# Kernel optimization log

Measured on AMD Instinct MI355X. Metric: run time of the kernel, lower is better.

## Reference

```python
import jax, jax.numpy as jnp
import numpy as np

N, E = 100_000, 1_600_000
C_IN = C_OUT = 2


def _ln(h, g, b, eps=1e-5):
    mu = h.mean(-1, keepdims=True)
    var = ((h - mu) ** 2).mean(-1, keepdims=True)
    return (h - mu) * jax.lax.rsqrt(var + eps) * g + b


def _radial(x, W1, b1, g1, be1, W2, b2, g2, be2, W3, b3):
    h = jax.nn.relu(_ln(x @ W1 + b1, g1, be1))
    h = jax.nn.relu(_ln(h @ W2 + b2, g2, be2))
    return h @ W3 + b3


def setup_inputs() -> dict:
    key = jax.random.key(0)
    ks = jax.random.split(key, 20)
    inp = {
        "f0": jax.random.normal(ks[0], (N, C_IN, 1), jnp.float32),
        "f1": jax.random.normal(ks[1], (N, C_IN, 3), jnp.float32),
        "dist": jax.random.uniform(ks[2], (E,), jnp.float32),
        "u": jax.random.randint(ks[3], (E,), 0, N),
        "v": jax.random.randint(ks[4], (E,), 0, N),
        "wq": 0.5 * jax.random.normal(ks[5], (2, C_OUT, C_IN), jnp.float32),
        "wj00": jax.random.normal(ks[6], (E, 1, 1, 1), jnp.float32),
        "wj01": jax.random.normal(ks[7], (E, 1, 1, 3), jnp.float32),
        "wj10": jax.random.normal(ks[8], (E, 1, 3, 1), jnp.float32),
        "wj11": jax.random.normal(ks[9], (E, 3, 3, 3), jnp.float32),
        # radial MLP params for the 4 WLayers, index i = 2*l + k
        "rW1": 0.5 * jax.random.normal(ks[10], (4, C_IN + 1, 16), jnp.float32),
        "rb1": jnp.zeros((4, 16), jnp.float32),
        "g1": jnp.ones((4, 16), jnp.float32),
        "be1": jnp.zeros((4, 16), jnp.float32),
        "rW2": 0.3 * jax.random.normal(ks[11], (4, 16, 16), jnp.float32),
        "rb2": jnp.zeros((4, 16), jnp.float32),
        "g2": jnp.ones((4, 16), jnp.float32),
        "be2": jnp.zeros((4, 16), jnp.float32),
        "W3_00": 0.3 * jax.random.normal(ks[12], (16, 4), jnp.float32),
        "b3_00": jnp.zeros((4,), jnp.float32),
        "W3_01": 0.3 * jax.random.normal(ks[13], (16, 4), jnp.float32),
        "b3_01": jnp.zeros((4,), jnp.float32),
        "W3_10": 0.3 * jax.random.normal(ks[14], (16, 4), jnp.float32),
        "b3_10": jnp.zeros((4,), jnp.float32),
        "W3_11": 0.3 * jax.random.normal(ks[15], (16, 12), jnp.float32),
        "b3_11": jnp.zeros((12,), jnp.float32),
    }
    return inp


def reference(f0, f1, dist, u, v, wq, wj00, wj01, wj10, wj11,
              rW1, rb1, g1, be1, rW2, rb2, g2, be2,
              W3_00, b3_00, W3_01, b3_01, W3_10, b3_10, W3_11, b3_11):
    n = f0.shape[0]
    e = u.shape[0]
    # calc_q: [N, c_out, sum(2k+1)=4]
    q = jnp.concatenate([jnp.einsum('oi,nik->nok', wq[0], f0),
                         jnp.einsum('oi,nik->nok', wq[1], f1)], axis=2)
    # per-edge radial input: [dot(f0_src, f0_dst) over rep dim, dist] -> [E, c_in+1]
    vec = jnp.concatenate([jnp.sum(f0[u] * f0[v], axis=2), dist[:, None]], axis=1)
    f_dst = (f0[v], f1[v])  # edges.dst[k]
    wjs = {(0, 0): wj00, (0, 1): wj01, (1, 0): wj10, (1, 1): wj11}
    W3s = {(0, 0): (W3_00, b3_00), (0, 1): (W3_01, b3_01),
           (1, 0): (W3_10, b3_10), (1, 1): (W3_11, b3_11)}
    # calc_k: for each output degree l, sum over input degrees k of
    #   einsum('ejoi,ejlk,eik->eol', R, w_j, f_dst[k])  (fused form of the
    #   original 'ejoi,ejlk->eoilk' then 'eoilk,eik->eol')
    kl = []
    for l in range(2):
        acc = jnp.zeros((e, C_OUT, 2 * l + 1), f0.dtype)
        for k in range(2):
            i = 2 * l + k
            W3, b3 = W3s[(l, k)]
            J = 2 * min(k, l) + 1
            R = _radial(vec, rW1[i], rb1[i], g1[i], be1[i],
                        rW2[i], rb2[i], g2[i], be2[i], W3, b3)
            R = R.reshape(e, J, C_OUT, C_IN)
            acc = acc + jnp.einsum('ejoi,ejlk,eik->eol', R, wjs[(l, k)], f_dst[k])
        kl.append(acc)
    k_feat = jnp.concatenate(kl, axis=2)  # [E, c_out, 4]
    dot = jnp.einsum('eol,eol->e', q[v], k_feat)  # [E]
    # scatter logsumexp over destination nodes, then edge softmax weights
    m = jax.lax.stop_gradient(jax.ops.segment_max(dot, v, num_segments=n))
    m = jnp.where(jnp.isfinite(m), m, 0.0)
    ssum = jax.ops.segment_sum(jnp.exp(dot - m[v]), v, num_segments=n)
    lse = m + jnp.log(ssum)
    return jnp.exp(dot - lse[v])
```

## Files before the change

kernel.cpp:

```cpp
#include <hip/hip_runtime.h>
#include <math.h>


#define TPB 256

typedef float f2 __attribute__((ext_vector_type(2)));

static __device__ __forceinline__ f2 fma2(f2 a, f2 b, f2 c) {
    return __builtin_elementwise_fma(a, b, c);
}
static __device__ __forceinline__ f2 splat(float x) {
    f2 r;
    r.x = x;
    r.y = x;
    return r;
}
static __device__ __forceinline__ float get16(const f2* h, int c) {
    return (c & 1) ? h[c >> 1].y : h[c >> 1].x;
}

static __device__ __forceinline__ void ln_relu16(f2* h, const float* __restrict__ g,
                                                 const float* __restrict__ be) {
    const f2* g2 = (const f2*)g;
    const f2* be2 = (const f2*)be;
    f2 s = h[0] + h[1] + h[2] + h[3] + h[4] + h[5] + h[6] + h[7];
    const float mu = (s.x + s.y) * 0.0625f;
    const f2 mu2 = splat(mu);
    f2 vs = splat(0.f);
#pragma unroll
    for (int i = 0; i < 8; ++i) {
        f2 d = h[i] - mu2;
        vs = fma2(d, d, vs);
    }
    const float var = (vs.x + vs.y) * 0.0625f;
    const f2 r2 = splat(rsqrtf(var + 1e-5f));
    const f2 zero = splat(0.f);
#pragma unroll
    for (int i = 0; i < 8; ++i) {
        f2 t = (h[i] - mu2) * r2;
        h[i] = __builtin_elementwise_max(fma2(t, g2[i], be2[i]), zero);
    }
}

static __device__ __forceinline__ void radial_h2(
    float v0, float v1, float v2, const float* __restrict__ W1,
    const float* __restrict__ b1, const float* __restrict__ g1,
    const float* __restrict__ be1, const float* __restrict__ W2,
    const float* __restrict__ b2, const float* __restrict__ g2,
    const float* __restrict__ be2, f2* h2) {
    const f2* W1r0 = (const f2*)W1;
    const f2* W1r1 = (const f2*)(W1 + 16);
    const f2* W1r2 = (const f2*)(W1 + 32);
    const f2* b1v = (const f2*)b1;
    const f2 a = splat(v0), b = splat(v1), c = splat(v2);
    f2 h[8];
#pragma unroll
    for (int j = 0; j < 8; ++j)
        h[j] = fma2(a, W1r0[j], fma2(b, W1r1[j], fma2(c, W1r2[j], b1v[j])));
    ln_relu16(h, g1, be1);

    const f2* b2v = (const f2*)b2;
#pragma unroll
    for (int j = 0; j < 8; ++j) h2[j] = b2v[j];
#pragma unroll
    for (int c16 = 0; c16 < 16; ++c16) {
        const f2 hc = splat(get16(h, c16));
        const f2* row = (const f2*)(W2 + c16 * 16);
#pragma unroll
        for (int j = 0; j < 8; ++j) h2[j] = fma2(hc, row[j], h2[j]);
    }
    ln_relu16(h2, g2, be2);
}

static __device__ __forceinline__ void layer3_4(const f2* h2,
                                                const float* __restrict__ W3,
                                                const float* __restrict__ b3,
                                                f2& p0, f2& p1) {
    p0 = *(const f2*)(b3);
    p1 = *(const f2*)(b3 + 2);
#pragma unroll
    for (int c = 0; c < 16; ++c) {
        const f2 hc = splat(get16(h2, c));
        p0 = fma2(hc, *(const f2*)(W3 + c * 4), p0);
        p1 = fma2(hc, *(const f2*)(W3 + c * 4 + 2), p1);
    }
}

__global__ __launch_bounds__(TPB, 2) void edge_kernel(
    const float* __restrict__ f0, const float* __restrict__ f1,
    const float* __restrict__ dist, const int* __restrict__ u,
    const int* __restrict__ v, const float* __restrict__ wq,
    const float* __restrict__ wj00, const float* __restrict__ wj01,
    const float* __restrict__ wj10, const float* __restrict__ wj11,
    const float* __restrict__ rW1, const float* __restrict__ rb1,
    const float* __restrict__ g1, const float* __restrict__ be1,
    const float* __restrict__ rW2, const float* __restrict__ rb2,
    const float* __restrict__ g2, const float* __restrict__ be2,
    const float* __restrict__ W3_00, const float* __restrict__ b3_00,
    const float* __restrict__ W3_01, const float* __restrict__ b3_01,
    const float* __restrict__ W3_10, const float* __restrict__ b3_10,
    const float* __restrict__ W3_11, const float* __restrict__ b3_11,
    float* __restrict__ out, double* __restrict__ ssum, int E) {
    int e = blockIdx.x * blockDim.x + threadIdx.x;
    if (e >= E) return;

    const int uu = u[e];
    const int vv = v[e];

    const float f0u0 = f0[uu * 2 + 0];
    const float f0u1 = f0[uu * 2 + 1];
    const float f0v0 = f0[vv * 2 + 0];
    const float f0v1 = f0[vv * 2 + 1];
    float f1v[2][3];
#pragma unroll
    for (int i = 0; i < 2; ++i)
#pragma unroll
        for (int m = 0; m < 3; ++m) f1v[i][m] = f1[vv * 6 + i * 3 + m];

    const float vec0 = f0u0 * f0v0;
    const float vec1 = f0u1 * f0v1;
    const float vec2 = dist[e];

    float acc0[2] = {0.f, 0.f};
    float acc1[2][3] = {{0.f, 0.f, 0.f}, {0.f, 0.f, 0.f}};

    {
        f2 h2[8];
        radial_h2(vec0, vec1, vec2, rW1 + 0 * 48, rb1 + 0 * 16, g1 + 0 * 16,
                  be1 + 0 * 16, rW2 + 0 * 256, rb2 + 0 * 16, g2 + 0 * 16,
                  be2 + 0 * 16, h2);
        f2 p0, p1;
        layer3_4(h2, W3_00, b3_00, p0, p1);
        const float w = wj00[e];
        acc0[0] += w * (p0.x * f0v0 + p0.y * f0v1);
        acc0[1] += w * (p1.x * f0v0 + p1.y * f0v1);
    }
    {
        f2 h2[8];
        radial_h2(vec0, vec1, vec2, rW1 + 1 * 48, rb1 + 1 * 16, g1 + 1 * 16,
                  be1 + 1 * 16, rW2 + 1 * 256, rb2 + 1 * 16, g2 + 1 * 16,
                  be2 + 1 * 16, h2);
        f2 p0, p1;
        layer3_4(h2, W3_01, b3_01, p0, p1);
        const float w0 = wj01[e * 3 + 0];
        const float w1 = wj01[e * 3 + 1];
        const float w2 = wj01[e * 3 + 2];
        const float s0 = w0 * f1v[0][0] + w1 * f1v[0][1] + w2 * f1v[0][2];
        const float s1 = w0 * f1v[1][0] + w1 * f1v[1][1] + w2 * f1v[1][2];
        acc0[0] += p0.x * s0 + p0.y * s1;
        acc0[1] += p1.x * s0 + p1.y * s1;
    }
    {
        f2 h2[8];
        radial_h2(vec0, vec1, vec2, rW1 + 2 * 48, rb1 + 2 * 16, g1 + 2 * 16,
                  be1 + 2 * 16, rW2 + 2 * 256, rb2 + 2 * 16, g2 + 2 * 16,
                  be2 + 2 * 16, h2);
        f2 p0, p1;
        layer3_4(h2, W3_10, b3_10, p0, p1);
        const float t0 = p0.x * f0v0 + p0.y * f0v1;
        const float t1 = p1.x * f0v0 + p1.y * f0v1;
#pragma unroll
        for (int m = 0; m < 3; ++m) {
            const float w = wj10[e * 3 + m];
            acc1[0][m] += w * t0;
            acc1[1][m] += w * t1;
        }
    }
    {
        f2 h2[8];
        radial_h2(vec0, vec1, vec2, rW1 + 3 * 48, rb1 + 3 * 16, g1 + 3 * 16,
                  be1 + 3 * 16, rW2 + 3 * 256, rb2 + 3 * 16, g2 + 3 * 16,
                  be2 + 3 * 16, h2);
#pragma unroll
        for (int j = 0; j < 3; ++j) {
            f2 p0 = *(const f2*)(b3_11 + j * 4);
            f2 p1 = *(const f2*)(b3_11 + j * 4 + 2);
#pragma unroll
            for (int c = 0; c < 16; ++c) {
                const f2 hc = splat(get16(h2, c));
                p0 = fma2(hc, *(const f2*)(W3_11 + c * 12 + j * 4), p0);
                p1 = fma2(hc, *(const f2*)(W3_11 + c * 12 + j * 4 + 2), p1);
            }
#pragma unroll
            for (int m = 0; m < 3; ++m) {
                const float w0 = wj11[e * 27 + j * 9 + m * 3 + 0];
                const float w1 = wj11[e * 27 + j * 9 + m * 3 + 1];
                const float w2 = wj11[e * 27 + j * 9 + m * 3 + 2];
                const float B0 =
                    w0 * f1v[0][0] + w1 * f1v[0][1] + w2 * f1v[0][2];
                const float B1 =
                    w0 * f1v[1][0] + w1 * f1v[1][1] + w2 * f1v[1][2];
                acc1[0][m] += p0.x * B0 + p0.y * B1;
                acc1[1][m] += p1.x * B0 + p1.y * B1;
            }
        }
    }

    float dot = 0.f;
    {
        const float q00 = wq[0] * f0v0 + wq[1] * f0v1;
        const float q01 = wq[2] * f0v0 + wq[3] * f0v1;
        dot += q00 * acc0[0] + q01 * acc0[1];
#pragma unroll
        for (int m = 0; m < 3; ++m) {
            const float q1m0 = wq[4] * f1v[0][m] + wq[5] * f1v[1][m];
            const float q1m1 = wq[6] * f1v[0][m] + wq[7] * f1v[1][m];
            dot += q1m0 * acc1[0][m] + q1m1 * acc1[1][m];
        }
    }

    out[e] = dot;
    atomicAdd(&ssum[vv], exp((double)dot));
}

__global__ void norm_kernel(float* __restrict__ out, const int* __restrict__ v,
                            const double* __restrict__ ssum, int E) {
    int e = blockIdx.x * blockDim.x + threadIdx.x;
    if (e >= E) return;
    const double t = exp((double)out[e]);
    out[e] = (float)(t / ssum[v[e]]);
}

extern "C" void kernel_launch(void* const* d_in, const int* in_sizes, int n_in,
                              void* d_out, int out_size, void* d_ws,
                              size_t ws_size, hipStream_t stream) {
    const float* f0 = (const float*)d_in[0];
    const float* f1 = (const float*)d_in[1];
    const float* dist = (const float*)d_in[2];
    const int* u = (const int*)d_in[3];
    const int* v = (const int*)d_in[4];
    const float* wq = (const float*)d_in[5];
    const float* wj00 = (const float*)d_in[6];
    const float* wj01 = (const float*)d_in[7];
    const float* wj10 = (const float*)d_in[8];
    const float* wj11 = (const float*)d_in[9];
    const float* rW1 = (const float*)d_in[10];
    const float* rb1 = (const float*)d_in[11];
    const float* g1 = (const float*)d_in[12];
    const float* be1 = (const float*)d_in[13];
    const float* rW2 = (const float*)d_in[14];
    const float* rb2 = (const float*)d_in[15];
    const float* g2 = (const float*)d_in[16];
    const float* be2 = (const float*)d_in[17];
    const float* W3_00 = (const float*)d_in[18];
    const float* b3_00 = (const float*)d_in[19];
    const float* W3_01 = (const float*)d_in[20];
    const float* b3_01 = (const float*)d_in[21];
    const float* W3_10 = (const float*)d_in[22];
    const float* b3_10 = (const float*)d_in[23];
    const float* W3_11 = (const float*)d_in[24];
    const float* b3_11 = (const float*)d_in[25];

    const int N = in_sizes[0] / 2;
    const int E = in_sizes[2];

    double* ssum = (double*)d_ws;
    float* out = (float*)d_out;

    const int ge = (E + TPB - 1) / TPB;

    hipMemsetAsync(ssum, 0, (size_t)N * sizeof(double), stream);
    edge_kernel<<<ge, TPB, 0, stream>>>(
        f0, f1, dist, u, v, wq, wj00, wj01, wj10, wj11, rW1, rb1, g1, be1, rW2,
        rb2, g2, be2, W3_00, b3_00, W3_01, b3_01, W3_10, b3_10, W3_11, b3_11,
        out, ssum, E);
    norm_kernel<<<ge, TPB, 0, stream>>>(out, v, ssum, E);
}
```

Baseline: 429.8 us.

## Roll radial MLPs into a loop, raise occupancy, cheaper wide exp, vectorize norm

Folds the four unrolled radial-MLP blocks into one non-unrolled loop with per-index branches, so code size and register pressure drop, and raises launch bounds to 4 blocks per CU. Replaces the double-precision exp with a float exp2 scaled by two double exponent factors, which keeps range without the costly f64 exp. Streaming inputs and outputs switch to nontemporal loads and stores. The norm kernel now handles two edges per thread with vector loads. Risks include branch overhead inside the loop, register spills under the tighter bound, and slight precision loss from the float-based exp.

```diff
diff --git a/kernel.cpp b/kernel.cpp
--- a/kernel.cpp
+++ b/kernel.cpp
@@ -5,6 +5,7 @@
 #define TPB 256
 
 typedef float f2 __attribute__((ext_vector_type(2)));
+typedef int i2 __attribute__((ext_vector_type(2)));
 
 static __device__ __forceinline__ f2 fma2(f2 a, f2 b, f2 c) {
     return __builtin_elementwise_fma(a, b, c);
@@ -17,6 +18,19 @@
 }
 static __device__ __forceinline__ float get16(const f2* h, int c) {
     return (c & 1) ? h[c >> 1].y : h[c >> 1].x;
+}
+
+static __device__ __forceinline__ double exp_wide(float d) {
+    d = fminf(fmaxf(d, -1400.f), 1400.f);
+    const float t = d * 1.44269504088896340736f;
+    const float k = rintf(t);
+    const float p = exp2f(t - k);
+    const int ik = (int)k;
+    const int k1 = ik >> 1;
+    const int k2 = ik - k1;
+    const double s1 = __hiloint2double((k1 + 1023) << 20, 0);
+    const double s2 = __hiloint2double((k2 + 1023) << 20, 0);
+    return ((double)p * s1) * s2;
 }
 
 static __device__ __forceinline__ void ln_relu16(f2* h, const float* __restrict__ g,
@@ -42,51 +56,7 @@
     }
 }
 
-static __device__ __forceinline__ void radial_h2(
-    float v0, float v1, float v2, const float* __restrict__ W1,
-    const float* __restrict__ b1, const float* __restrict__ g1,
-    const float* __restrict__ be1, const float* __restrict__ W2,
-    const float* __restrict__ b2, const float* __restrict__ g2,
-    const float* __restrict__ be2, f2* h2) {
-    const f2* W1r0 = (const f2*)W1;
-    const f2* W1r1 = (const f2*)(W1 + 16);
-    const f2* W1r2 = (const f2*)(W1 + 32);
-    const f2* b1v = (const f2*)b1;
-    const f2 a = splat(v0), b = splat(v1), c = splat(v2);
-    f2 h[8];
-#pragma unroll
-    for (int j = 0; j < 8; ++j)
-        h[j] = fma2(a, W1r0[j], fma2(b, W1r1[j], fma2(c, W1r2[j], b1v[j])));
-    ln_relu16(h, g1, be1);
-
-    const f2* b2v = (const f2*)b2;
-#pragma unroll
-    for (int j = 0; j < 8; ++j) h2[j] = b2v[j];
-#pragma unroll
-    for (int c16 = 0; c16 < 16; ++c16) {
-        const f2 hc = splat(get16(h, c16));
-        const f2* row = (const f2*)(W2 + c16 * 16);
-#pragma unroll
-        for (int j = 0; j < 8; ++j) h2[j] = fma2(hc, row[j], h2[j]);
-    }
-    ln_relu16(h2, g2, be2);
-}
-
-static __device__ __forceinline__ void layer3_4(const f2* h2,
-                                                const float* __restrict__ W3,
-                                                const float* __restrict__ b3,
-                                                f2& p0, f2& p1) {
-    p0 = *(const f2*)(b3);
-    p1 = *(const f2*)(b3 + 2);
-#pragma unroll
-    for (int c = 0; c < 16; ++c) {
-        const f2 hc = splat(get16(h2, c));
-        p0 = fma2(hc, *(const f2*)(W3 + c * 4), p0);
-        p1 = fma2(hc, *(const f2*)(W3 + c * 4 + 2), p1);
-    }
-}
-
-__global__ __launch_bounds__(TPB, 2) void edge_kernel(
+__global__ __launch_bounds__(TPB, 4) void edge_kernel(
     const float* __restrict__ f0, const float* __restrict__ f1,
     const float* __restrict__ dist, const int* __restrict__ u,
     const int* __restrict__ v, const float* __restrict__ wq,
@@ -101,10 +71,10 @@
     const float* __restrict__ W3_10, const float* __restrict__ b3_10,
     const float* __restrict__ W3_11, const float* __restrict__ b3_11,
     float* __restrict__ out, double* __restrict__ ssum, int E) {
-    int e = blockIdx.x * blockDim.x + threadIdx.x;
+    const int e = blockIdx.x * blockDim.x + threadIdx.x;
     if (e >= E) return;
 
-    const int uu = u[e];
+    const int uu = __builtin_nontemporal_load(u + e);
     const int vv = v[e];
 
     const float f0u0 = f0[uu * 2 + 0];
@@ -119,79 +89,123 @@
 
     const float vec0 = f0u0 * f0v0;
     const float vec1 = f0u1 * f0v1;
-    const float vec2 = dist[e];
+    const float vec2 = __builtin_nontemporal_load(dist + e);
 
     float acc0[2] = {0.f, 0.f};
     float acc1[2][3] = {{0.f, 0.f, 0.f}, {0.f, 0.f, 0.f}};
 
-    {
+#pragma clang loop unroll(disable)
+    for (int i = 0; i < 4; ++i) {
+        const float* W1 = rW1 + i * 48;
+        const float* b1 = rb1 + i * 16;
+        const float* g1i = g1 + i * 16;
+        const float* be1i = be1 + i * 16;
+        const float* W2 = rW2 + i * 256;
+        const float* b2 = rb2 + i * 16;
+        const float* g2i = g2 + i * 16;
+        const float* be2i = be2 + i * 16;
+
+        f2 h[8];
+        {
+            const f2* W1r0 = (const f2*)W1;
+            const f2* W1r1 = (const f2*)(W1 + 16);
+            const f2* W1r2 = (const f2*)(W1 + 32);
+            const f2* b1v = (const f2*)b1;
+            const f2 a = splat(vec0), b = splat(vec1), c = splat(vec2);
+#pragma unroll
+            for (int j = 0; j < 8; ++j)
+                h[j] = fma2(a, W1r0[j],
+                            fma2(b, W1r1[j], fma2(c, W1r2[j], b1v[j])));
+        }
+        ln_relu16(h, g1i, be1i);
+
         f2 h2[8];
-        radial_h2(vec0, vec1, vec2, rW1 + 0 * 48, rb1 + 0 * 16, g1 + 0 * 16,
-                  be1 + 0 * 16, rW2 + 0 * 256, rb2 + 0 * 16, g2 + 0 * 16,
-                  be2 + 0 * 16, h2);
-        f2 p0, p1;
-        layer3_4(h2, W3_00, b3_00, p0, p1);
-        const float w = wj00[e];
-        acc0[0] += w * (p0.x * f0v0 + p0.y * f0v1);
-        acc0[1] += w * (p1.x * f0v0 + p1.y * f0v1);
-    }
-    {
-        f2 h2[8];
-        radial_h2(vec0, vec1, vec2, rW1 + 1 * 48, rb1 + 1 * 16, g1 + 1 * 16,
-                  be1 + 1 * 16, rW2 + 1 * 256, rb2 + 1 * 16, g2 + 1 * 16,
-                  be2 + 1 * 16, h2);
-        f2 p0, p1;
-        layer3_4(h2, W3_01, b3_01, p0, p1);
-        const float w0 = wj01[e * 3 + 0];
-        const float w1 = wj01[e * 3 + 1];
-        const float w2 = wj01[e * 3 + 2];
-        const float s0 = w0 * f1v[0][0] + w1 * f1v[0][1] + w2 * f1v[0][2];
-        const float s1 = w0 * f1v[1][0] + w1 * f1v[1][1] + w2 * f1v[1][2];
-        acc0[0] += p0.x * s0 + p0.y * s1;
-        acc0[1] += p1.x * s0 + p1.y * s1;
-    }
-    {
-        f2 h2[8];
-        radial_h2(vec0, vec1, vec2, rW1 + 2 * 48, rb1 + 2 * 16, g1 + 2 * 16,
-                  be1 + 2 * 16, rW2 + 2 * 256, rb2 + 2 * 16, g2 + 2 * 16,
-                  be2 + 2 * 16, h2);
-        f2 p0, p1;
-        layer3_4(h2, W3_10, b3_10, p0, p1);
-        const float t0 = p0.x * f0v0 + p0.y * f0v1;
-        const float t1 = p1.x * f0v0 + p1.y * f0v1;
-#pragma unroll
-        for (int m = 0; m < 3; ++m) {
-            const float w = wj10[e * 3 + m];
-            acc1[0][m] += w * t0;
-            acc1[1][m] += w * t1;
-        }
-    }
-    {
-        f2 h2[8];
-        radial_h2(vec0, vec1, vec2, rW1 + 3 * 48, rb1 + 3 * 16, g1 + 3 * 16,
-                  be1 + 3 * 16, rW2 + 3 * 256, rb2 + 3 * 16, g2 + 3 * 16,
-                  be2 + 3 * 16, h2);
-#pragma unroll
-        for (int j = 0; j < 3; ++j) {
-            f2 p0 = *(const f2*)(b3_11 + j * 4);
-            f2 p1 = *(const f2*)(b3_11 + j * 4 + 2);
+        {
+            const f2* b2v = (const f2*)b2;
+#pragma unroll
+            for (int j = 0; j < 8; ++j) h2[j] = b2v[j];
+#pragma unroll
+            for (int c = 0; c < 16; ++c) {
+                const f2 hc = splat(get16(h, c));
+                const f2* row = (const f2*)(W2 + c * 16);
+#pragma unroll
+                for (int j = 0; j < 8; ++j) h2[j] = fma2(hc, row[j], h2[j]);
+            }
+        }
+        ln_relu16(h2, g2i, be2i);
+
+        if (i == 3) {
+#pragma unroll
+            for (int j = 0; j < 3; ++j) {
+                f2 p0 = *(const f2*)(b3_11 + j * 4);
+                f2 p1 = *(const f2*)(b3_11 + j * 4 + 2);
+#pragma unroll
+                for (int c = 0; c < 16; ++c) {
+                    const f2 hc = splat(get16(h2, c));
+                    p0 = fma2(hc, *(const f2*)(W3_11 + c * 12 + j * 4), p0);
+                    p1 = fma2(hc, *(const f2*)(W3_11 + c * 12 + j * 4 + 2), p1);
+                }
+#pragma unroll
+                for (int m = 0; m < 3; ++m) {
+                    const float w0 = __builtin_nontemporal_load(
+                        wj11 + e * 27 + j * 9 + m * 3 + 0);
+                    const float w1 = __builtin_nontemporal_load(
+                        wj11 + e * 27 + j * 9 + m * 3 + 1);
+                    const float w2 = __builtin_nontemporal_load(
+                        wj11 + e * 27 + j * 9 + m * 3 + 2);
+                    const float B0 =
+                        w0 * f1v[0][0] + w1 * f1v[0][1] + w2 * f1v[0][2];
+                    const float B1 =
+                        w0 * f1v[1][0] + w1 * f1v[1][1] + w2 * f1v[1][2];
+                    acc1[0][m] += p0.x * B0 + p0.y * B1;
+                    acc1[1][m] += p1.x * B0 + p1.y * B1;
+                }
+            }
+        } else {
+            const float* W3p;
+            const float* b3p;
+            if (i == 0) {
+                W3p = W3_00;
+                b3p = b3_00;
+            } else if (i == 1) {
+                W3p = W3_01;
+                b3p = b3_01;
+            } else {
+                W3p = W3_10;
+                b3p = b3_10;
+            }
+            f2 p0 = *(const f2*)(b3p);
+            f2 p1 = *(const f2*)(b3p + 2);
 #pragma unroll
             for (int c = 0; c < 16; ++c) {
                 const f2 hc = splat(get16(h2, c));
-                p0 = fma2(hc, *(const f2*)(W3_11 + c * 12 + j * 4), p0);
-                p1 = fma2(hc, *(const f2*)(W3_11 + c * 12 + j * 4 + 2), p1);
-            }
-#pragma unroll
-            for (int m = 0; m < 3; ++m) {
-                const float w0 = wj11[e * 27 + j * 9 + m * 3 + 0];
-                const float w1 = wj11[e * 27 + j * 9 + m * 3 + 1];
-                const float w2 = wj11[e * 27 + j * 9 + m * 3 + 2];
-                const float B0 =
+                p0 = fma2(hc, *(const f2*)(W3p + c * 4), p0);
+                p1 = fma2(hc, *(const f2*)(W3p + c * 4 + 2), p1);
+            }
+            if (i == 0) {
+                const float w = __builtin_nontemporal_load(wj00 + e);
+                acc0[0] += w * (p0.x * f0v0 + p0.y * f0v1);
+                acc0[1] += w * (p1.x * f0v0 + p1.y * f0v1);
+            } else if (i == 1) {
+                const float w0 = __builtin_nontemporal_load(wj01 + e * 3 + 0);
+                const float w1 = __builtin_nontemporal_load(wj01 + e * 3 + 1);
+                const float w2 = __builtin_nontemporal_load(wj01 + e * 3 + 2);
+                const float s0 =
                     w0 * f1v[0][0] + w1 * f1v[0][1] + w2 * f1v[0][2];
-                const float B1 =
+                const float s1 =
                     w0 * f1v[1][0] + w1 * f1v[1][1] + w2 * f1v[1][2];
-                acc1[0][m] += p0.x * B0 + p0.y * B1;
-                acc1[1][m] += p1.x * B0 + p1.y * B1;
+                acc0[0] += p0.x * s0 + p0.y * s1;
+                acc0[1] += p1.x * s0 + p1.y * s1;
+            } else {
+                const float t0 = p0.x * f0v0 + p0.y * f0v1;
+                const float t1 = p1.x * f0v0 + p1.y * f0v1;
+#pragma unroll
+                for (int m = 0; m < 3; ++m) {
+                    const float w =
+                        __builtin_nontemporal_load(wj10 + e * 3 + m);
+                    acc1[0][m] += w * t0;
+                    acc1[1][m] += w * t1;
+                }
             }
         }
     }
@@ -209,16 +223,27 @@
         }
     }
 
-    out[e] = dot;
-    atomicAdd(&ssum[vv], exp((double)dot));
+    __builtin_nontemporal_store(dot, out + e);
+    atomicAdd(&ssum[vv], exp_wide(dot));
 }
 
 __global__ void norm_kernel(float* __restrict__ out, const int* __restrict__ v,
                             const double* __restrict__ ssum, int E) {
-    int e = blockIdx.x * blockDim.x + threadIdx.x;
-    if (e >= E) return;
-    const double t = exp((double)out[e]);
-    out[e] = (float)(t / ssum[v[e]]);
+    const int t = blockIdx.x * blockDim.x + threadIdx.x;
+    const int e0 = t * 2;
+    if (e0 >= E) return;
+    if (e0 + 1 < E) {
+        const f2 dv = *((const f2*)out + t);
+        const i2 vv = *((const i2*)v + t);
+        const double s0 = ssum[vv.x];
+        const double s1 = ssum[vv.y];
+        f2 r;
+        r.x = (float)(exp_wide(dv.x) / s0);
+        r.y = (float)(exp_wide(dv.y) / s1);
+        __builtin_nontemporal_store(r, (f2*)out + t);
+    } else {
+        out[e0] = (float)(exp_wide(out[e0]) / ssum[v[e0]]);
+    }
 }
 
 extern "C" void kernel_launch(void* const* d_in, const int* in_sizes, int n_in,
@@ -258,11 +283,12 @@
     float* out = (float*)d_out;
 
     const int ge = (E + TPB - 1) / TPB;
+    const int gp = ((E + 1) / 2 + TPB - 1) / TPB;
 
     hipMemsetAsync(ssum, 0, (size_t)N * sizeof(double), stream);
     edge_kernel<<<ge, TPB, 0, stream>>>(
         f0, f1, dist, u, v, wq, wj00, wj01, wj10, wj11, rW1, rb1, g1, be1, rW2,
         rb2, g2, be2, W3_00, b3_00, W3_01, b3_01, W3_10, b3_10, W3_11, b3_11,
         out, ssum, E);
-    norm_kernel<<<ge, TPB, 0, stream>>>(out, v, ssum, E);
-}
+    norm_kernel<<<gp, TPB, 0, stream>>>(out, v, ssum, E);
+}
```

Result: slower. 450.5 us (+4.8%).
